# Optimization experiments

Hardware: AMD Instinct MI355X
Metric: run time of the kernel (lower is better)

Reference implementation:

```python
import jax, jax.numpy as jnp
import numpy as np

N, E, H, G, C = 50000, 800000, 512, 64, 2
BERT = 768


def setup_inputs() -> dict:
    key = jax.random.key(0)
    ks = jax.random.split(key, 12)
    sem = jax.random.normal(ks[0], (N, BERT), jnp.float32)
    mask = jax.random.randint(ks[1], (N, 1), 0, 2).astype(jnp.float32)
    x = jnp.concatenate([sem, mask], axis=1)  # [N, 769]
    edge_index = jax.random.randint(ks[2], (2, E), 0, N)
    batch = jnp.sort(jax.random.randint(ks[3], (N,), 0, G))
    s = lambda k, shp, fan: jax.random.normal(k, shp, jnp.float32) / np.float32(np.sqrt(fan))
    return dict(
        x=x, edge_index=edge_index, batch=batch,
        sem_W=s(ks[4], (BERT, H), BERT), sem_b=jnp.zeros((H,), jnp.float32),
        slice_emb=jax.random.normal(ks[5], (2, H), jnp.float32),
        ln_g=jnp.ones((H,), jnp.float32), ln_b=jnp.zeros((H,), jnp.float32),
        conv1_W=s(ks[6], (H, H), H), conv1_b=jnp.zeros((H,), jnp.float32),
        conv2_W=s(ks[7], (H, H), H), conv2_b=jnp.zeros((H,), jnp.float32),
        cls_W1=s(ks[8], (H, H), H), cls_b1=jnp.zeros((H,), jnp.float32),
        cls_W2=s(ks[9], (H, C), H), cls_b2=jnp.zeros((C,), jnp.float32),
    )


def _layer_norm(x, g, b, eps=1e-5):
    m = x.mean(-1, keepdims=True)
    v = x.var(-1, keepdims=True)
    return (x - m) * jax.lax.rsqrt(v + eps) * g + b


def _gcn_conv(h, src, dst, W, b):
    # PyG GCNConv: add self-loops, sym-normalized aggregation of X @ W, plus bias
    hw = h @ W  # [N, H]
    deg = jnp.zeros((N,), hw.dtype).at[dst].add(1.0) + 1.0  # +1 self-loop
    dinv = jax.lax.rsqrt(deg)
    coef = dinv[src] * dinv[dst]  # [E]
    agg = jax.ops.segment_sum(hw[src] * coef[:, None], dst, num_segments=N)
    agg = agg + hw * (dinv * dinv)[:, None]  # self-loop contribution
    return agg + b


def reference(x, edge_index, batch, sem_W, sem_b, slice_emb, ln_g, ln_b,
              conv1_W, conv1_b, conv2_W, conv2_b, cls_W1, cls_b1, cls_W2, cls_b2):
    sem = x[:, :BERT]
    idx = x[:, BERT].astype(jnp.int32)  # binary slice mask
    h = sem @ sem_W + sem_b + slice_emb[idx]
    h = jax.nn.gelu(_layer_norm(h, ln_g, ln_b), approximate=False)
    src, dst = edge_index[0], edge_index[1]
    h = jax.nn.gelu(_gcn_conv(h, src, dst, conv1_W, conv1_b), approximate=False)
    h2 = jax.nn.gelu(_gcn_conv(h, src, dst, conv2_W, conv2_b), approximate=False)
    h = h + h2  # residual (args.residual=True)
    sums = jax.ops.segment_sum(h, batch, num_segments=G)
    cnt = jax.ops.segment_sum(jnp.ones((N,), h.dtype), batch, num_segments=G)
    hg = sums / jnp.maximum(cnt, 1.0)[:, None]  # global mean pool [G, H]
    z = jax.nn.gelu(hg @ cls_W1 + cls_b1, approximate=False)
    return z @ cls_W2 + cls_b2  # [G, C]
```

## Files before the change

kernel.cpp:

```cpp
#include <hip/hip_runtime.h>
#include <hip/hip_bf16.h>

typedef unsigned short u16;
typedef __bf16 bfv8 __attribute__((ext_vector_type(8)));
typedef float f32x4 __attribute__((ext_vector_type(4)));
typedef unsigned int u32x4 __attribute__((ext_vector_type(4)));

#define HH 512
#define BERT_D 768
#define XSTRIDE 769
#define BM 128
#define BN 256
#define BK 64

__device__ __forceinline__ float gelu_f(float x) {
  return 0.5f * x * (1.0f + erff(x * 0.70710678118654752440f));
}
__device__ __forceinline__ float us2f(u16 u) {
  union { unsigned int i; float f; } c; c.i = ((unsigned int)u) << 16; return c.f;
}
__device__ __forceinline__ u16 f2us(float f) {
  union { float f; unsigned int i; } c; c.f = f;
  unsigned int i = c.i;
  i += 0x7FFFu + ((i >> 16) & 1u);
  return (u16)(i >> 16);
}
__device__ __forceinline__ void gl_lds16(const u16* g, u16* l) {
  __builtin_amdgcn_global_load_lds((const __attribute__((address_space(1))) void*)g,
                                   (__attribute__((address_space(3))) void*)l, 16, 0, 0);
}

__global__ void k_idx(const float* __restrict__ x, int* __restrict__ idx, int Nn) {
  int i = blockIdx.x * blockDim.x + threadIdx.x;
  if (i < Nn) idx[i] = (int)x[(size_t)i * XSTRIDE + BERT_D];
}

__global__ void k_transpose_bf16(const float* __restrict__ src, u16* __restrict__ dst,
                                 int K, int Nn) {
  int i = blockIdx.x * blockDim.x + threadIdx.x;
  if (i >= K * Nn) return;
  int k = i / Nn, j = i - k * Nn;
  dst[(size_t)j * K + k] = f2us(src[i]);
}

__global__ void k_deg(const int* __restrict__ dst, int* __restrict__ deg, int E) {
  int e = blockIdx.x * blockDim.x + threadIdx.x;
  if (e < E) atomicAdd(&deg[dst[e]], 1);
}

__launch_bounds__(256)
__global__ void k_part(const int* __restrict__ deg, int* __restrict__ part, int Nn) {
  const int i = blockIdx.x * 256 + threadIdx.x;
  int v = (i < Nn) ? deg[i] : 0;
#pragma unroll
  for (int o = 32; o; o >>= 1) v += __shfl_xor(v, o);
  __shared__ int ws4[4];
  if ((threadIdx.x & 63) == 0) ws4[threadIdx.x >> 6] = v;
  __syncthreads();
  if (threadIdx.x == 0) part[blockIdx.x] = ws4[0] + ws4[1] + ws4[2] + ws4[3];
}

__launch_bounds__(256)
__global__ void k_scan_part(int* __restrict__ part, int* __restrict__ row_ptr,
                            int nb, int Nn) {
  __shared__ int sm[256];
  const int t = threadIdx.x;
  int v = (t < nb) ? part[t] : 0;
  sm[t] = v;
  __syncthreads();
  for (int d = 1; d < 256; d <<= 1) {
    int u = (t >= d) ? sm[t - d] : 0;
    __syncthreads();
    sm[t] += u;
    __syncthreads();
  }
  if (t < nb) part[t] = sm[t] - v;
  if (t == 255) row_ptr[Nn] = sm[255];
}

__launch_bounds__(256)
__global__ void k_scan_write(const int* __restrict__ deg, const int* __restrict__ part,
                             int* __restrict__ row_ptr, int* __restrict__ cursor,
                             float* __restrict__ dinv, int Nn) {
  __shared__ int sm[256];
  const int t = threadIdx.x;
  const int i = blockIdx.x * 256 + t;
  int v = (i < Nn) ? deg[i] : 0;
  sm[t] = v;
  __syncthreads();
  for (int d = 1; d < 256; d <<= 1) {
    int u = (t >= d) ? sm[t - d] : 0;
    __syncthreads();
    sm[t] += u;
    __syncthreads();
  }
  if (i < Nn) {
    int pre = part[blockIdx.x] + sm[t] - v;
    row_ptr[i] = pre;
    cursor[i] = pre;
    dinv[i] = rsqrtf((float)v + 1.0f);
  }
}

__global__ void k_csr(const int* __restrict__ src, const int* __restrict__ dst,
                      int* __restrict__ cursor, int* __restrict__ csr_src, int E) {
  int e = blockIdx.x * blockDim.x + threadIdx.x;
  if (e >= E) return;
  int d = dst[e];
  int pos = atomicAdd(&cursor[d], 1);
  csr_src[pos] = src[e];
}


__launch_bounds__(512, 2)
__global__ void k_gemm1(const float* __restrict__ xf,
                        const u16* __restrict__ B, int ldb,
                        u16* __restrict__ C, int M,
                        const float* __restrict__ bias,
                        const float* __restrict__ emb,
                        const int* __restrict__ idx) {
  __shared__ alignas(16) u16 As[2][BM * BK];
  __shared__ alignas(16) u16 Bs[2][BN * BK];
  const int t = threadIdx.x;
  const int l = t & 63;
  const int w = t >> 6;
  const int wro = (w >> 2) * 64;
  const int wco = (w & 3) * 64;
  const int lr = l & 15;
  const int kq = l >> 4;
  const int rsw = lr & 7;
  const int nwg = gridDim.x;
  const int id = blockIdx.x;
  const int q8 = nwg >> 3, r8 = nwg & 7;
  const int xcd = id & 7, rk = id >> 3;
  const int swz = (xcd < r8 ? xcd * (q8 + 1) : r8 * (q8 + 1) + (xcd - r8) * q8) + rk;
  const int brow = (swz >> 1) * BM;
  const int bcol = (swz & 1) * BN;

  const int ssw8 = (((t & 7) ^ ((t >> 3) & 7)) * 8);
  const int arow = t >> 2;
  const int ag0 = (t & 3) * 2;
  const int arsw = arow & 7;

  int agr = brow + arow; if (agr > M - 1) agr = M - 1;
  const float* xrow = xf + (size_t)agr * XSTRIDE;

  float av[16];

  f32x4 acc[4][4] = {};

  auto stageB = [&](int k0, int buf) {
#pragma unroll
    for (int i = 0; i < 4; ++i) {
      const int r = i * 64 + (t >> 3);
      gl_lds16(B + (size_t)(bcol + r) * ldb + (k0 + ssw8), &Bs[buf][(i * 512 + t) * 8]);
    }
  };
  auto loadA = [&](int k0) {
#pragma unroll
    for (int j = 0; j < 2; ++j) {
      const int sg = (ag0 + j) ^ arsw;
      const float* xp = xrow + k0 + sg * 8;
#pragma unroll
      for (int e = 0; e < 8; ++e) av[j * 8 + e] = xp[e];
    }
  };
  auto writeA = [&](int buf) {
#pragma unroll
    for (int j = 0; j < 2; ++j) {
      union { u16 h[8]; uint4 q; } pk;
#pragma unroll
      for (int e = 0; e < 8; ++e) pk.h[e] = f2us(av[j * 8 + e]);
      *(uint4*)(&As[buf][arow * 64 + (ag0 + j) * 8]) = pk.q;
    }
  };

  loadA(0);
  stageB(0, 0);
  writeA(0);
  __syncthreads();

  int cur = 0;
  for (int st = 0; st < BERT_D / BK; ++st) {
    const bool hn = (st + 1 < BERT_D / BK);
    if (hn) { loadA((st + 1) * BK); stageB((st + 1) * BK, cur ^ 1); }
    const u16* Ac = As[cur];
    const u16* Bc = Bs[cur];
#pragma unroll
    for (int ks = 0; ks < 2; ++ks) {
      bfv8 af[4], bfr[4];
      const int rg = ((ks * 4 + kq) ^ rsw) * 8;
#pragma unroll
      for (int m = 0; m < 4; ++m)
        af[m] = __builtin_bit_cast(bfv8, *(const uint4*)(Ac + (wro + m * 16 + lr) * 64 + rg));
#pragma unroll
      for (int n = 0; n < 4; ++n)
        bfr[n] = __builtin_bit_cast(bfv8, *(const uint4*)(Bc + (wco + n * 16 + lr) * 64 + rg));
#pragma unroll
      for (int m = 0; m < 4; ++m)
#pragma unroll
        for (int n = 0; n < 4; ++n)
          acc[m][n] = __builtin_amdgcn_mfma_f32_16x16x32_bf16(af[m], bfr[n], acc[m][n], 0, 0, 0);
    }
    if (hn) writeA(cur ^ 1);
    __syncthreads();
    cur ^= 1;
  }

#pragma unroll
  for (int m = 0; m < 4; ++m) {
#pragma unroll
    for (int r = 0; r < 4; ++r) {
      const int row = brow + wro + m * 16 + (l >> 4) * 4 + r;
      if (row >= M) continue;
#pragma unroll
      for (int n = 0; n < 4; ++n) {
        const int col = bcol + wco + n * 16 + lr;
        float v = acc[m][n][r] + bias[col] + emb[idx[row] * HH + col];
        C[(size_t)row * HH + col] = f2us(v);
      }
    }
  }
}

template <int EPI>
__launch_bounds__(512, 2)
__global__ void k_gemm_bt(const u16* __restrict__ A, int lda,
                          const u16* __restrict__ B, int ldb,
                          u16* __restrict__ C, int M, int Kd,
                          const float* __restrict__ dscale) {
  __shared__ alignas(16) u16 As[2][BM * BK];
  __shared__ alignas(16) u16 Bs[2][BN * BK];
  const int t = threadIdx.x;
  const int l = t & 63;
  const int w = t >> 6;
  const int wro = (w >> 2) * 64;
  const int wco = (w & 3) * 64;
  const int lr = l & 15;
  const int kq = l >> 4;
  const int rsw = lr & 7;
  const int nwg = gridDim.x;
  const int id = blockIdx.x;
  const int q8 = nwg >> 3, r8 = nwg & 7;
  const int xcd = id & 7, rk = id >> 3;
  const int swz = (xcd < r8 ? xcd * (q8 + 1) : r8 * (q8 + 1) + (xcd - r8) * q8) + rk;
  const int brow = (swz >> 1) * BM;
  const int bcol = (swz & 1) * BN;

  const int ssw8 = (((t & 7) ^ ((t >> 3) & 7)) * 8);
  const int srow = t >> 3;

  f32x4 acc[4][4] = {};

  auto stage = [&](int k0, int buf) {
#pragma unroll
    for (int i = 0; i < 2; ++i) {
      const int r = i * 64 + srow;
      int gr = brow + r; if (gr > M - 1) gr = M - 1;
      gl_lds16(A + (size_t)gr * lda + (k0 + ssw8), &As[buf][(i * 512 + t) * 8]);
    }
#pragma unroll
    for (int i = 0; i < 4; ++i) {
      const int r = i * 64 + srow;
      gl_lds16(B + (size_t)(bcol + r) * ldb + (k0 + ssw8), &Bs[buf][(i * 512 + t) * 8]);
    }
  };

  stage(0, 0);
  __syncthreads();

  const int nst = Kd / BK;
  int cur = 0;
  for (int st = 0; st < nst; ++st) {
    if (st + 1 < nst) stage((st + 1) * BK, cur ^ 1);
    const u16* Ac = As[cur];
    const u16* Bc = Bs[cur];
#pragma unroll
    for (int ks = 0; ks < 2; ++ks) {
      bfv8 af[4], bfr[4];
      const int rg = ((ks * 4 + kq) ^ rsw) * 8;
#pragma unroll
      for (int m = 0; m < 4; ++m)
        af[m] = __builtin_bit_cast(bfv8, *(const uint4*)(Ac + (wro + m * 16 + lr) * 64 + rg));
#pragma unroll
      for (int n = 0; n < 4; ++n)
        bfr[n] = __builtin_bit_cast(bfv8, *(const uint4*)(Bc + (wco + n * 16 + lr) * 64 + rg));
#pragma unroll
      for (int m = 0; m < 4; ++m)
#pragma unroll
        for (int n = 0; n < 4; ++n)
          acc[m][n] = __builtin_amdgcn_mfma_f32_16x16x32_bf16(af[m], bfr[n], acc[m][n], 0, 0, 0);
    }
    __syncthreads();
    cur ^= 1;
  }

#pragma unroll
  for (int m = 0; m < 4; ++m) {
#pragma unroll
    for (int r = 0; r < 4; ++r) {
      const int row = brow + wro + m * 16 + (l >> 4) * 4 + r;
      if (row >= M) continue;
      const float sc = (EPI == 2) ? dscale[row] : 1.0f;
#pragma unroll
      for (int n = 0; n < 4; ++n) {
        const int col = bcol + wco + n * 16 + lr;
        float v = acc[m][n][r];
        if (EPI == 2) v *= sc;
        C[(size_t)row * HH + col] = f2us(v);
      }
    }
  }
}

__launch_bounds__(256)
__global__ void k_ln_gelu(const u16* __restrict__ h0, const float* __restrict__ gw,
                          const float* __restrict__ bw, u16* __restrict__ hout, int Nn) {
  const int wid = (int)((blockIdx.x * (long long)blockDim.x + threadIdx.x) >> 6);
  if (wid >= Nn) return;
  const int l = threadIdx.x & 63;
  uint4 q = *(const uint4*)(h0 + (size_t)wid * HH + l * 8);
  const u16* us = (const u16*)&q;
  float f[8]; float s = 0.f, s2 = 0.f;
#pragma unroll
  for (int j = 0; j < 8; ++j) { f[j] = us2f(us[j]); s += f[j]; s2 += f[j] * f[j]; }
#pragma unroll
  for (int o = 32; o; o >>= 1) { s += __shfl_xor(s, o); s2 += __shfl_xor(s2, o); }
  const float mean = s * (1.f / 512.f);
  const float var = s2 * (1.f / 512.f) - mean * mean;
  const float rs = rsqrtf(var + 1e-5f);
  union { u16 ov[8]; uint4 q; } o;
#pragma unroll
  for (int j = 0; j < 8; ++j) {
    int col = l * 8 + j;
    float y = (f[j] - mean) * rs * gw[col] + bw[col];
    o.ov[j] = f2us(gelu_f(y));
  }
  *(uint4*)(hout + (size_t)wid * HH + l * 8) = o.q;
}

__launch_bounds__(256)
__global__ void k_agg(const u16* __restrict__ hwS, const int* __restrict__ row_ptr,
                      const int* __restrict__ csr_src, const float* __restrict__ dinv,
                      const float* __restrict__ bias, u16* __restrict__ hout, int Nn) {
  const int wid = (int)((blockIdx.x * (long long)blockDim.x + threadIdx.x) >> 6);
  if (wid >= Nn) return;
  const int l = threadIdx.x & 63;
  const int cb = l * 8;
  float acc[8] = {0.f, 0.f, 0.f, 0.f, 0.f, 0.f, 0.f, 0.f};
  const int lo = row_ptr[wid], hi = row_ptr[wid + 1];
  const float dv = dinv[wid];
  int e = lo;
  for (; e + 4 <= hi; e += 4) {
    const int u0 = csr_src[e + 0];
    const int u1 = csr_src[e + 1];
    const int u2 = csr_src[e + 2];
    const int u3 = csr_src[e + 3];
    uint4 q0 = *(const uint4*)(hwS + (size_t)u0 * HH + cb);
    uint4 q1 = *(const uint4*)(hwS + (size_t)u1 * HH + cb);
    uint4 q2 = *(const uint4*)(hwS + (size_t)u2 * HH + cb);
    uint4 q3 = *(const uint4*)(hwS + (size_t)u3 * HH + cb);
    const u16* p0 = (const u16*)&q0;
    const u16* p1 = (const u16*)&q1;
    const u16* p2 = (const u16*)&q2;
    const u16* p3 = (const u16*)&q3;
#pragma unroll
    for (int j = 0; j < 8; ++j)
      acc[j] += (us2f(p0[j]) + us2f(p1[j])) + (us2f(p2[j]) + us2f(p3[j]));
  }
  for (; e < hi; ++e) {
    const int u = csr_src[e];
    uint4 q = *(const uint4*)(hwS + (size_t)u * HH + cb);
    const u16* p = (const u16*)&q;
#pragma unroll
    for (int j = 0; j < 8; ++j) acc[j] += us2f(p[j]);
  }
  {
    uint4 q = *(const uint4*)(hwS + (size_t)wid * HH + cb);
    const u16* p = (const u16*)&q;
#pragma unroll
    for (int j = 0; j < 8; ++j) acc[j] += us2f(p[j]);
  }
  union { u16 ov[8]; u32x4 q; } o;
#pragma unroll
  for (int j = 0; j < 8; ++j) {
    float v = acc[j] * dv + bias[cb + j];
    o.ov[j] = f2us(gelu_f(v));
  }
  __builtin_nontemporal_store(o.q, (u32x4*)(hout + (size_t)wid * HH + cb));
}

#define POOL_RS 16
__launch_bounds__(256)
__global__ void k_pool2(const u16* __restrict__ h1, const u16* __restrict__ h2,
                        const int* __restrict__ batch, float* __restrict__ hg, int Nn) {
  const int g = blockIdx.x;
  const int chunk = blockIdx.y;
  const int t = threadIdx.x;
  const int w = t >> 6;
  const int l = t & 63;
  const int cb = l * 8;
  int lo, hi;
  { int a = 0, b = Nn; while (a < b) { int m = (a + b) >> 1; if (batch[m] < g) a = m + 1; else b = m; } lo = a; }
  { int a = 0, b = Nn; while (a < b) { int m = (a + b) >> 1; if (batch[m] < g + 1) a = m + 1; else b = m; } hi = a; }
  const int len = hi - lo;
  const int per = (len + POOL_RS - 1) / POOL_RS;
  const int rlo = lo + chunk * per;
  const int rhi = min(rlo + per, hi);
  float acc[8] = {};
  for (int r = rlo + w; r < rhi; r += 4) {
    u32x4 a = __builtin_nontemporal_load((const u32x4*)(h1 + (size_t)r * HH + cb));
    u32x4 b = __builtin_nontemporal_load((const u32x4*)(h2 + (size_t)r * HH + cb));
    const u16* ua = (const u16*)&a;
    const u16* ub = (const u16*)&b;
#pragma unroll
    for (int j = 0; j < 8; ++j) acc[j] += us2f(ua[j]) + us2f(ub[j]);
  }
  __shared__ float red[4][HH];
#pragma unroll
  for (int j = 0; j < 8; ++j) red[w][cb + j] = acc[j];
  __syncthreads();
  if (w == 0) {
#pragma unroll
    for (int j = 0; j < 8; ++j) {
      const int col = cb + j;
      float s = red[0][col] + red[1][col] + red[2][col] + red[3][col];
      if (s != 0.f) atomicAdd(&hg[(size_t)g * HH + col], s);
    }
  }
}

__launch_bounds__(256)
__global__ void k_cls(const float* __restrict__ hg, const int* __restrict__ batch,
                      const float* __restrict__ W1, const float* __restrict__ b1,
                      const float* __restrict__ W2, const float* __restrict__ b2,
                      float* __restrict__ out, int Nn) {
  const int g = blockIdx.x;
  const int t = threadIdx.x;
  __shared__ float hl[512];
  __shared__ float zl[512];
  __shared__ float pr[512];
  int lo, hi;
  { int a = 0, b = Nn; while (a < b) { int m = (a + b) >> 1; if (batch[m] < g) a = m + 1; else b = m; } lo = a; }
  { int a = 0, b = Nn; while (a < b) { int m = (a + b) >> 1; if (batch[m] < g + 1) a = m + 1; else b = m; } hi = a; }
  const float inv = 1.0f / fmaxf((float)(hi - lo), 1.0f);
  hl[t] = hg[(size_t)g * HH + t] * inv;
  hl[t + 256] = hg[(size_t)g * HH + t + 256] * inv;
  __syncthreads();
#pragma unroll
  for (int jj = 0; jj < 2; ++jj) {
    const int j = t + jj * 256;
    float a = b1[j];
    for (int k = 0; k < 512; ++k) a += hl[k] * W1[k * HH + j];
    zl[j] = gelu_f(a);
  }
  __syncthreads();
  float p0 = 0.f, p1 = 0.f;
  for (int k = t; k < 512; k += 256) { p0 += zl[k] * W2[k * 2]; p1 += zl[k] * W2[k * 2 + 1]; }
  pr[t] = p0; pr[t + 256] = p1;
  __syncthreads();
  for (int s2 = 128; s2; s2 >>= 1) {
    if (t < s2) { pr[t] += pr[t + s2]; pr[t + 256] += pr[t + 256 + s2]; }
    __syncthreads();
  }
  if (t == 0) { out[g * 2] = pr[0] + b2[0]; out[g * 2 + 1] = pr[256] + b2[1]; }
}

extern "C" void kernel_launch(void* const* d_in, const int* in_sizes, int n_in,
                              void* d_out, int out_size, void* d_ws, size_t ws_size,
                              hipStream_t stream) {
  const float* x        = (const float*)d_in[0];
  const int*   eidx     = (const int*)d_in[1];
  const int*   batch    = (const int*)d_in[2];
  const float* sem_W    = (const float*)d_in[3];
  const float* sem_b    = (const float*)d_in[4];
  const float* sl_emb   = (const float*)d_in[5];
  const float* ln_g     = (const float*)d_in[6];
  const float* ln_b     = (const float*)d_in[7];
  const float* W1       = (const float*)d_in[8];
  const float* b1       = (const float*)d_in[9];
  const float* W2       = (const float*)d_in[10];
  const float* b2       = (const float*)d_in[11];
  const float* cW1      = (const float*)d_in[12];
  const float* cb1      = (const float*)d_in[13];
  const float* cW2      = (const float*)d_in[14];
  const float* cb2      = (const float*)d_in[15];
  const int N_ = in_sizes[2];
  const int E_ = in_sizes[1] / 2;
  const int G_ = out_size / 2;
  const int* src = eidx;
  const int* dst = eidx + E_;

  char* ws = (char*)d_ws;
  size_t off = 0;
  auto alloc = [&](size_t bytes) -> void* {
    void* p = (void*)(ws + off);
    off += (bytes + 255) & ~(size_t)255;
    return p;
  };
  u16* h1 = (u16*)alloc((size_t)N_ * HH * sizeof(u16));
  u16* h0 = (u16*)alloc((size_t)N_ * HH * sizeof(u16));
  u16* hw = h0;
  u16* h = (u16*)alloc((size_t)N_ * HH * sizeof(u16));
  u16* h2 = h;
  u16* semW_T = (u16*)alloc((size_t)HH * BERT_D * sizeof(u16));
  u16* W1T    = (u16*)alloc((size_t)HH * HH * sizeof(u16));
  u16* W2T    = (u16*)alloc((size_t)HH * HH * sizeof(u16));
  int* idx     = (int*)alloc((size_t)N_ * 4);
  int* deg     = (int*)alloc((size_t)N_ * 4);
  float* dinv  = (float*)alloc((size_t)N_ * 4);
  int* row_ptr = (int*)alloc((size_t)(N_ + 1) * 4);
  int* cursor  = (int*)alloc((size_t)N_ * 4);
  int* csr_src = (int*)alloc((size_t)E_ * 4);
  int* part    = (int*)alloc(1024);
  float* hg    = (float*)alloc((size_t)G_ * HH * 4);

  hipMemsetAsync(deg, 0, (size_t)N_ * 4, stream);
  hipMemsetAsync(hg, 0, (size_t)G_ * HH * 4, stream);

  k_idx<<<(N_ + 255) / 256, 256, 0, stream>>>(x, idx, N_);
  k_transpose_bf16<<<(BERT_D * HH + 255) / 256, 256, 0, stream>>>(sem_W, semW_T, BERT_D, HH);
  k_transpose_bf16<<<(HH * HH + 255) / 256, 256, 0, stream>>>(W1, W1T, HH, HH);
  k_transpose_bf16<<<(HH * HH + 255) / 256, 256, 0, stream>>>(W2, W2T, HH, HH);

  const int nb = (N_ + 255) / 256;
  k_deg<<<(E_ + 255) / 256, 256, 0, stream>>>(dst, deg, E_);
  k_part<<<nb, 256, 0, stream>>>(deg, part, N_);
  k_scan_part<<<1, 256, 0, stream>>>(part, row_ptr, nb, N_);
  k_scan_write<<<nb, 256, 0, stream>>>(deg, part, row_ptr, cursor, dinv, N_);
  k_csr<<<(E_ + 255) / 256, 256, 0, stream>>>(src, dst, cursor, csr_src, E_);

  const int Mtiles = (N_ + BM - 1) / BM;
  const int wave_blocks = (N_ + 3) / 4;
  const int gemm_grid = Mtiles * (HH / BN);

  k_gemm1<<<gemm_grid, 512, 0, stream>>>(
      x, semW_T, BERT_D, h0, N_, sem_b, sl_emb, idx);
  k_ln_gelu<<<wave_blocks, 256, 0, stream>>>(h0, ln_g, ln_b, h, N_);
  k_gemm_bt<2><<<gemm_grid, 512, 0, stream>>>(
      h, HH, W1T, HH, hw, N_, HH, dinv);
  k_agg<<<wave_blocks, 256, 0, stream>>>(hw, row_ptr, csr_src, dinv, b1, h1, N_);
  k_gemm_bt<2><<<gemm_grid, 512, 0, stream>>>(
      h1, HH, W2T, HH, hw, N_, HH, dinv);
  k_agg<<<wave_blocks, 256, 0, stream>>>(hw, row_ptr, csr_src, dinv, b2, h2, N_);
  k_pool2<<<dim3(G_, POOL_RS), 256, 0, stream>>>(h1, h2, batch, hg, N_);
  k_cls<<<G_, 256, 0, stream>>>(hg, batch, cW1, cb1, cW2, cb2, (float*)d_out, N_);
}
```

Measured before the change: 782.0 us.

## Shrink GEMM tiles to 64x256 with 4 waves and explicit waitcnt pipelining

Halves the GEMM row tile to 64 and uses 256-thread blocks where each of the 4 waves owns a 64-column slice, which doubles the grid and is meant to improve load balance and occupancy. Each k-step now uses explicit s_waitcnt vmcnt/lgkmcnt counts and raw s_barrier in place of __syncthreads, so the next stage's global-to-LDS loads can stay in flight while the current stage computes. The A-tile loader in the first GEMM is reorganized to match the new staging layout. In exchange, each B tile is reloaded by twice as many blocks, and the hand-tuned wait counts are fragile if the load count per stage changes.

```diff
diff --git a/kernel.cpp b/kernel.cpp
--- a/kernel.cpp
+++ b/kernel.cpp
@@ -9,9 +9,12 @@
 #define HH 512
 #define BERT_D 768
 #define XSTRIDE 769
-#define BM 128
+#define BM 64
 #define BN 256
 #define BK 64
+
+#define FENCE asm volatile("" ::: "memory")
+#define SBAR  do { FENCE; __builtin_amdgcn_s_barrier(); FENCE; } while (0)
 
 __device__ __forceinline__ float gelu_f(float x) {
   return 0.5f * x * (1.0f + erff(x * 0.70710678118654752440f));
@@ -112,7 +115,102 @@
 }
 
 
-__launch_bounds__(512, 2)
+template <int EPI>
+__launch_bounds__(256, 2)
+__global__ void k_gemm_bt(const u16* __restrict__ A, int lda,
+                          const u16* __restrict__ B, int ldb,
+                          u16* __restrict__ C, int M, int Kd,
+                          const float* __restrict__ dscale) {
+  __shared__ alignas(16) u16 As[2][BM * BK];
+  __shared__ alignas(16) u16 Bs[2][BN * BK];
+  const int t = threadIdx.x;
+  const int l = t & 63;
+  const int w = t >> 6;
+  const int wco = w * 64;
+  const int lr = l & 15;
+  const int kq = l >> 4;
+  const int rsw = lr & 7;
+  const int nwg = gridDim.x;
+  const int id = blockIdx.x;
+  const int q8 = nwg >> 3, r8 = nwg & 7;
+  const int xcd = id & 7, rk = id >> 3;
+  const int swz = (xcd < r8 ? xcd * (q8 + 1) : r8 * (q8 + 1) + (xcd - r8) * q8) + rk;
+  const int brow = (swz >> 1) * BM;
+  const int bcol = (swz & 1) * BN;
+
+  const int ssw8 = (((t & 7) ^ ((t >> 3) & 7)) * 8);
+  const int sr = t >> 3;
+
+  f32x4 acc[4][4] = {};
+
+  auto stage = [&](int k0, int buf) {
+#pragma unroll
+    for (int i = 0; i < 2; ++i) {
+      int gr = brow + i * 32 + sr; if (gr > M - 1) gr = M - 1;
+      gl_lds16(A + (size_t)gr * lda + (k0 + ssw8), &As[buf][(i * 256 + t) * 8]);
+    }
+#pragma unroll
+    for (int i = 0; i < 8; ++i) {
+      const int r = i * 32 + sr;
+      gl_lds16(B + (size_t)(bcol + r) * ldb + (k0 + ssw8), &Bs[buf][(i * 256 + t) * 8]);
+    }
+  };
+
+  auto compute = [&](int buf) {
+#pragma unroll
+    for (int ks = 0; ks < 2; ++ks) {
+      bfv8 af[4], bfr[4];
+      const int rg = ((ks * 4 + kq) ^ rsw) * 8;
+#pragma unroll
+      for (int m = 0; m < 4; ++m)
+        af[m] = __builtin_bit_cast(bfv8, *(const uint4*)(&As[buf][(m * 16 + lr) * 64 + rg]));
+#pragma unroll
+      for (int n = 0; n < 4; ++n)
+        bfr[n] = __builtin_bit_cast(bfv8, *(const uint4*)(&Bs[buf][(wco + n * 16 + lr) * 64 + rg]));
+#pragma unroll
+      for (int m = 0; m < 4; ++m)
+#pragma unroll
+        for (int n = 0; n < 4; ++n)
+          acc[m][n] = __builtin_amdgcn_mfma_f32_16x16x32_bf16(af[m], bfr[n], acc[m][n], 0, 0, 0);
+    }
+  };
+
+  stage(0, 0);
+  const int nst = Kd / BK;
+  int cur = 0;
+  for (int st = 0; st < nst; ++st) {
+    if (st + 1 < nst) {
+      stage((st + 1) * BK, cur ^ 1);
+      asm volatile("s_waitcnt vmcnt(10)" ::: "memory");
+    } else {
+      asm volatile("s_waitcnt vmcnt(0)" ::: "memory");
+    }
+    SBAR;
+    compute(cur);
+    asm volatile("s_waitcnt lgkmcnt(0)" ::: "memory");
+    SBAR;
+    cur ^= 1;
+  }
+
+#pragma unroll
+  for (int m = 0; m < 4; ++m) {
+#pragma unroll
+    for (int r = 0; r < 4; ++r) {
+      const int row = brow + m * 16 + (l >> 4) * 4 + r;
+      if (row >= M) continue;
+      const float sc = (EPI == 2) ? dscale[row] : 1.0f;
+#pragma unroll
+      for (int n = 0; n < 4; ++n) {
+        const int col = bcol + wco + n * 16 + lr;
+        float v = acc[m][n][r];
+        if (EPI == 2) v *= sc;
+        C[(size_t)row * HH + col] = f2us(v);
+      }
+    }
+  }
+}
+
+__launch_bounds__(256, 2)
 __global__ void k_gemm1(const float* __restrict__ xf,
                         const u16* __restrict__ B, int ldb,
                         u16* __restrict__ C, int M,
@@ -124,8 +222,7 @@
   const int t = threadIdx.x;
   const int l = t & 63;
   const int w = t >> 6;
-  const int wro = (w >> 2) * 64;
-  const int wco = (w & 3) * 64;
+  const int wco = w * 64;
   const int lr = l & 15;
   const int kq = l >> 4;
   const int rsw = lr & 7;
@@ -138,72 +235,86 @@
   const int bcol = (swz & 1) * BN;
 
   const int ssw8 = (((t & 7) ^ ((t >> 3) & 7)) * 8);
-  const int arow = t >> 2;
-  const int ag0 = (t & 3) * 2;
-  const int arsw = arow & 7;
-
-  int agr = brow + arow; if (agr > M - 1) agr = M - 1;
-  const float* xrow = xf + (size_t)agr * XSTRIDE;
-
-  float av[16];
-
-  f32x4 acc[4][4] = {};
-
+  const int sr = t >> 3;
+
+  int ar0 = brow + sr;        if (ar0 > M - 1) ar0 = M - 1;
+  int ar1 = brow + 32 + sr;   if (ar1 > M - 1) ar1 = M - 1;
+  const float* xr0 = xf + (size_t)ar0 * XSTRIDE + ssw8;
+  const float* xr1 = xf + (size_t)ar1 * XSTRIDE + ssw8;
+
+  float av[2][8];
+
+  auto loadA = [&](int k0) {
+#pragma unroll
+    for (int e = 0; e < 8; ++e) av[0][e] = xr0[k0 + e];
+#pragma unroll
+    for (int e = 0; e < 8; ++e) av[1][e] = xr1[k0 + e];
+  };
   auto stageB = [&](int k0, int buf) {
 #pragma unroll
-    for (int i = 0; i < 4; ++i) {
-      const int r = i * 64 + (t >> 3);
-      gl_lds16(B + (size_t)(bcol + r) * ldb + (k0 + ssw8), &Bs[buf][(i * 512 + t) * 8]);
-    }
-  };
-  auto loadA = [&](int k0) {
-#pragma unroll
-    for (int j = 0; j < 2; ++j) {
-      const int sg = (ag0 + j) ^ arsw;
-      const float* xp = xrow + k0 + sg * 8;
-#pragma unroll
-      for (int e = 0; e < 8; ++e) av[j * 8 + e] = xp[e];
-    }
-  };
-  auto writeA = [&](int buf) {
-#pragma unroll
-    for (int j = 0; j < 2; ++j) {
+    for (int i = 0; i < 8; ++i) {
+      const int r = i * 32 + sr;
+      gl_lds16(B + (size_t)(bcol + r) * ldb + (k0 + ssw8), &Bs[buf][(i * 256 + t) * 8]);
+    }
+  };
+  auto packA = [&](int buf) {
+#pragma unroll
+    for (int i = 0; i < 2; ++i) {
       union { u16 h[8]; uint4 q; } pk;
 #pragma unroll
-      for (int e = 0; e < 8; ++e) pk.h[e] = f2us(av[j * 8 + e]);
-      *(uint4*)(&As[buf][arow * 64 + (ag0 + j) * 8]) = pk.q;
-    }
-  };
-
-  loadA(0);
-  stageB(0, 0);
-  writeA(0);
-  __syncthreads();
-
-  int cur = 0;
-  for (int st = 0; st < BERT_D / BK; ++st) {
-    const bool hn = (st + 1 < BERT_D / BK);
-    if (hn) { loadA((st + 1) * BK); stageB((st + 1) * BK, cur ^ 1); }
-    const u16* Ac = As[cur];
-    const u16* Bc = Bs[cur];
+      for (int e = 0; e < 8; ++e) pk.h[e] = f2us(av[i][e]);
+      *(uint4*)(&As[buf][(i * 256 + t) * 8]) = pk.q;
+    }
+  };
+
+  auto compute = [&](int buf, f32x4 (&acc)[4][4]) {
 #pragma unroll
     for (int ks = 0; ks < 2; ++ks) {
       bfv8 af[4], bfr[4];
       const int rg = ((ks * 4 + kq) ^ rsw) * 8;
 #pragma unroll
       for (int m = 0; m < 4; ++m)
-        af[m] = __builtin_bit_cast(bfv8, *(const uint4*)(Ac + (wro + m * 16 + lr) * 64 + rg));
+        af[m] = __builtin_bit_cast(bfv8, *(const uint4*)(&As[buf][(m * 16 + lr) * 64 + rg]));
 #pragma unroll
       for (int n = 0; n < 4; ++n)
-        bfr[n] = __builtin_bit_cast(bfv8, *(const uint4*)(Bc + (wco + n * 16 + lr) * 64 + rg));
+        bfr[n] = __builtin_bit_cast(bfv8, *(const uint4*)(&Bs[buf][(wco + n * 16 + lr) * 64 + rg]));
 #pragma unroll
       for (int m = 0; m < 4; ++m)
 #pragma unroll
         for (int n = 0; n < 4; ++n)
           acc[m][n] = __builtin_amdgcn_mfma_f32_16x16x32_bf16(af[m], bfr[n], acc[m][n], 0, 0, 0);
     }
-    if (hn) writeA(cur ^ 1);
-    __syncthreads();
+  };
+
+  f32x4 acc[4][4] = {};
+
+  loadA(0);
+  FENCE;
+  stageB(0, 0);
+  packA(0);
+  asm volatile("s_waitcnt lgkmcnt(0)" ::: "memory");
+
+  const int nst = BERT_D / BK;
+  int cur = 0;
+  for (int st = 0; st < nst; ++st) {
+    const bool hn = (st + 1 < nst);
+    if (hn) {
+      stageB((st + 1) * BK, cur ^ 1);
+      FENCE;
+      loadA((st + 1) * BK);
+      asm volatile("s_waitcnt vmcnt(8)" ::: "memory");
+    } else {
+      asm volatile("s_waitcnt vmcnt(0)" ::: "memory");
+    }
+    SBAR;
+    compute(cur, acc);
+    if (hn) {
+      packA(cur ^ 1);
+      asm volatile("s_waitcnt lgkmcnt(0)" ::: "memory");
+    } else {
+      asm volatile("s_waitcnt lgkmcnt(0)" ::: "memory");
+    }
+    SBAR;
     cur ^= 1;
   }
 
@@ -211,102 +322,12 @@
   for (int m = 0; m < 4; ++m) {
 #pragma unroll
     for (int r = 0; r < 4; ++r) {
-      const int row = brow + wro + m * 16 + (l >> 4) * 4 + r;
+      const int row = brow + m * 16 + (l >> 4) * 4 + r;
       if (row >= M) continue;
 #pragma unroll
       for (int n = 0; n < 4; ++n) {
         const int col = bcol + wco + n * 16 + lr;
         float v = acc[m][n][r] + bias[col] + emb[idx[row] * HH + col];
-        C[(size_t)row * HH + col] = f2us(v);
-      }
-    }
-  }
-}
-
-template <int EPI>
-__launch_bounds__(512, 2)
-__global__ void k_gemm_bt(const u16* __restrict__ A, int lda,
-                          const u16* __restrict__ B, int ldb,
-                          u16* __restrict__ C, int M, int Kd,
-                          const float* __restrict__ dscale) {
-  __shared__ alignas(16) u16 As[2][BM * BK];
-  __shared__ alignas(16) u16 Bs[2][BN * BK];
-  const int t = threadIdx.x;
-  const int l = t & 63;
-  const int w = t >> 6;
-  const int wro = (w >> 2) * 64;
-  const int wco = (w & 3) * 64;
-  const int lr = l & 15;
-  const int kq = l >> 4;
-  const int rsw = lr & 7;
-  const int nwg = gridDim.x;
-  const int id = blockIdx.x;
-  const int q8 = nwg >> 3, r8 = nwg & 7;
-  const int xcd = id & 7, rk = id >> 3;
-  const int swz = (xcd < r8 ? xcd * (q8 + 1) : r8 * (q8 + 1) + (xcd - r8) * q8) + rk;
-  const int brow = (swz >> 1) * BM;
-  const int bcol = (swz & 1) * BN;
-
-  const int ssw8 = (((t & 7) ^ ((t >> 3) & 7)) * 8);
-  const int srow = t >> 3;
-
-  f32x4 acc[4][4] = {};
-
-  auto stage = [&](int k0, int buf) {
-#pragma unroll
-    for (int i = 0; i < 2; ++i) {
-      const int r = i * 64 + srow;
-      int gr = brow + r; if (gr > M - 1) gr = M - 1;
-      gl_lds16(A + (size_t)gr * lda + (k0 + ssw8), &As[buf][(i * 512 + t) * 8]);
-    }
-#pragma unroll
-    for (int i = 0; i < 4; ++i) {
-      const int r = i * 64 + srow;
-      gl_lds16(B + (size_t)(bcol + r) * ldb + (k0 + ssw8), &Bs[buf][(i * 512 + t) * 8]);
-    }
-  };
-
-  stage(0, 0);
-  __syncthreads();
-
-  const int nst = Kd / BK;
-  int cur = 0;
-  for (int st = 0; st < nst; ++st) {
-    if (st + 1 < nst) stage((st + 1) * BK, cur ^ 1);
-    const u16* Ac = As[cur];
-    const u16* Bc = Bs[cur];
-#pragma unroll
-    for (int ks = 0; ks < 2; ++ks) {
-      bfv8 af[4], bfr[4];
-      const int rg = ((ks * 4 + kq) ^ rsw) * 8;
-#pragma unroll
-      for (int m = 0; m < 4; ++m)
-        af[m] = __builtin_bit_cast(bfv8, *(const uint4*)(Ac + (wro + m * 16 + lr) * 64 + rg));
-#pragma unroll
-      for (int n = 0; n < 4; ++n)
-        bfr[n] = __builtin_bit_cast(bfv8, *(const uint4*)(Bc + (wco + n * 16 + lr) * 64 + rg));
-#pragma unroll
-      for (int m = 0; m < 4; ++m)
-#pragma unroll
-        for (int n = 0; n < 4; ++n)
-          acc[m][n] = __builtin_amdgcn_mfma_f32_16x16x32_bf16(af[m], bfr[n], acc[m][n], 0, 0, 0);
-    }
-    __syncthreads();
-    cur ^= 1;
-  }
-
-#pragma unroll
-  for (int m = 0; m < 4; ++m) {
-#pragma unroll
-    for (int r = 0; r < 4; ++r) {
-      const int row = brow + wro + m * 16 + (l >> 4) * 4 + r;
-      if (row >= M) continue;
-      const float sc = (EPI == 2) ? dscale[row] : 1.0f;
-#pragma unroll
-      for (int n = 0; n < 4; ++n) {
-        const int col = bcol + wco + n * 16 + lr;
-        float v = acc[m][n][r];
-        if (EPI == 2) v *= sc;
         C[(size_t)row * HH + col] = f2us(v);
       }
     }
@@ -534,13 +555,13 @@
   const int wave_blocks = (N_ + 3) / 4;
   const int gemm_grid = Mtiles * (HH / BN);
 
-  k_gemm1<<<gemm_grid, 512, 0, stream>>>(
+  k_gemm1<<<gemm_grid, 256, 0, stream>>>(
       x, semW_T, BERT_D, h0, N_, sem_b, sl_emb, idx);
   k_ln_gelu<<<wave_blocks, 256, 0, stream>>>(h0, ln_g, ln_b, h, N_);
-  k_gemm_bt<2><<<gemm_grid, 512, 0, stream>>>(
+  k_gemm_bt<2><<<gemm_grid, 256, 0, stream>>>(
       h, HH, W1T, HH, hw, N_, HH, dinv);
   k_agg<<<wave_blocks, 256, 0, stream>>>(hw, row_ptr, csr_src, dinv, b1, h1, N_);
-  k_gemm_bt<2><<<gemm_grid, 512, 0, stream>>>(
+  k_gemm_bt<2><<<gemm_grid, 256, 0, stream>>>(
       h1, HH, W2T, HH, hw, N_, HH, dinv);
   k_agg<<<wave_blocks, 256, 0, stream>>>(hw, row_ptr, csr_src, dinv, b2, h2, N_);
   k_pool2<<<dim3(G_, POOL_RS), 256, 0, stream>>>(h1, h2, batch, hg, N_);
```

After: 748.3 us. 1.05x faster.
